# Performance work log

Hardware: AMD Instinct MI355X
Metric: run time of the kernel (lower is better)

Reference implementation:

```python
import jax, jax.numpy as jnp
import numpy as np

H = 1024
R = 16


def setup_inputs() -> dict:
    key = jax.random.key(0)
    ks = jax.random.split(key, 9)
    s = 1.0 / np.sqrt(H)
    x = jax.random.normal(ks[0], (8192, H), dtype=jnp.float32)
    # gate (rule_attention): Linear(H, R)
    Wa = jax.random.uniform(ks[1], (H, R), minval=-s, maxval=s, dtype=jnp.float32)
    ba = jax.random.uniform(ks[2], (R,), minval=-s, maxval=s, dtype=jnp.float32)
    # stacked rule_heads: R x (Linear(H,H) -> ReLU -> Linear(H,H))
    W1 = jax.random.uniform(ks[3], (R, H, H), minval=-s, maxval=s, dtype=jnp.float32)
    b1 = jax.random.uniform(ks[4], (R, H), minval=-s, maxval=s, dtype=jnp.float32)
    W2 = jax.random.uniform(ks[5], (R, H, H), minval=-s, maxval=s, dtype=jnp.float32)
    b2 = jax.random.uniform(ks[6], (R, H), minval=-s, maxval=s, dtype=jnp.float32)
    # stacked rule_confidence: R x (Linear(H,1) -> Sigmoid)
    Wc = jax.random.uniform(ks[7], (R, H), minval=-s, maxval=s, dtype=jnp.float32)
    bc = jax.random.uniform(ks[8], (R,), minval=-s, maxval=s, dtype=jnp.float32)
    return {"x": x, "Wa": Wa, "ba": ba, "W1": W1, "b1": b1,
            "W2": W2, "b2": b2, "Wc": Wc, "bc": bc}


def reference(x, Wa, ba, W1, b1, W2, b2, Wc, bc):
    # gate: softmax over rules               [B, R]
    attention = jax.nn.softmax(x @ Wa + ba, axis=-1)
    # all rule MLPs as one batched matmul    [B, R, H]
    h = jax.nn.relu(jnp.einsum("bh,rhd->brd", x, W1) + b1)
    outputs = jnp.einsum("brd,rdo->bro", h, W2) + b2
    # per-rule confidence                    [B, R]
    confidences = jax.nn.sigmoid(jnp.einsum("bh,rh->br", x, Wc) + bc)
    # combine gate with confidence, renormalize, weighted sum over rules
    combined = attention * confidences
    combined = combined / (combined.sum(axis=-1, keepdims=True) + 1e-8)
    output = jnp.einsum("bro,br->bo", outputs, combined)  # [B, H]
    return output, confidences
```

## Files before the change

kernel.cpp:

```cpp
#include <hip/hip_runtime.h>

typedef __attribute__((ext_vector_type(8))) short short8;
typedef __attribute__((ext_vector_type(4))) float f32x4;

#define B_SZ 8192
#define H_SZ 1024
#define R_SZ 16

__device__ __forceinline__ unsigned short f2bf(float f) {
  union { float f; unsigned u; } v; v.f = f;
  unsigned u = v.u + 0x7FFFu + ((v.u >> 16) & 1u);
  return (unsigned short)(u >> 16);
}

__global__ __launch_bounds__(256) void tck_transpose(const float* __restrict__ src,
                                                     unsigned short* __restrict__ dst,
                                                     int rows, int cols) {
  __shared__ float t[32][33];
  size_t zoff = (size_t)blockIdx.z * (size_t)rows * cols;
  int c0 = blockIdx.x * 32, r0 = blockIdx.y * 32;
  int tx = threadIdx.x, ty = threadIdx.y;
#pragma unroll
  for (int i = 0; i < 4; ++i)
    t[ty + 8 * i][tx] = src[zoff + (size_t)(r0 + ty + 8 * i) * cols + c0 + tx];
  __syncthreads();
#pragma unroll
  for (int i = 0; i < 4; ++i)
    dst[zoff + (size_t)(c0 + ty + 8 * i) * rows + r0 + tx] = f2bf(t[tx][ty + 8 * i]);
}

__global__ __launch_bounds__(256) void twk_transpose_wa(const float* __restrict__ Wa,
                                                        float* __restrict__ WaT) {
  int t = blockIdx.x * 256 + threadIdx.x;
  int h = t >> 4, r = t & 15;
  WaT[r * H_SZ + h] = Wa[t];
}

__global__ __launch_bounds__(256) void gk_gate(const float* __restrict__ x,
                                               const float* __restrict__ WaT,
                                               const float* __restrict__ ba,
                                               const float* __restrict__ Wc,
                                               const float* __restrict__ bc,
                                               float* __restrict__ comb,
                                               float* __restrict__ conf,
                                               unsigned short* __restrict__ xb) {
  int b = blockIdx.x * 4 + (threadIdx.x >> 6);
  int l = threadIdx.x & 63;
  const float* xr = x + (size_t)b * H_SZ;
  unsigned short* xbr = xb + (size_t)b * H_SZ;
  float xv[16];
#pragma unroll
  for (int j = 0; j < 16; ++j) xv[j] = xr[l + 64 * j];
#pragma unroll
  for (int j = 0; j < 16; ++j) xbr[l + 64 * j] = f2bf(xv[j]);
  float la[16], lcf[16];
#pragma unroll
  for (int r = 0; r < 16; ++r) {
    float sa = 0.f, sc = 0.f;
#pragma unroll
    for (int j = 0; j < 16; ++j) {
      int h = l + 64 * j;
      sa += xv[j] * WaT[r * H_SZ + h];
      sc += xv[j] * Wc[r * H_SZ + h];
    }
#pragma unroll
    for (int off = 32; off > 0; off >>= 1) {
      sa += __shfl_xor(sa, off);
      sc += __shfl_xor(sc, off);
    }
    la[r] = sa + ba[r];
    lcf[r] = sc + bc[r];
  }
  float mx = la[0];
#pragma unroll
  for (int r = 1; r < 16; ++r) mx = fmaxf(mx, la[r]);
  float se = 0.f;
#pragma unroll
  for (int r = 0; r < 16; ++r) { la[r] = expf(la[r] - mx); se += la[r]; }
  float cb[16]; float cs = 0.f;
#pragma unroll
  for (int r = 0; r < 16; ++r) {
    float cf = 1.f / (1.f + expf(-lcf[r]));
    lcf[r] = cf;
    cb[r] = (la[r] / se) * cf;
    cs += cb[r];
  }
  float inv = 1.f / (cs + 1e-8f);
  if (l < 16) {
    float cv = 0.f, qv = 0.f;
#pragma unroll
    for (int r = 0; r < 16; ++r)
      if (r == l) { cv = lcf[r]; qv = cb[r] * inv; }
    conf[b * 16 + l] = cv;
    comb[b * 16 + l] = qv;
  }
}

__device__ __forceinline__ void gload16(const unsigned short* g, const unsigned short* l) {
  __builtin_amdgcn_global_load_lds(
      (const __attribute__((address_space(1))) unsigned int*)g,
      (__attribute__((address_space(3))) unsigned int*)(unsigned short*)l, 16, 0, 0);
}

#define RDA(DST, MH)                                                                   \
  _Pragma("unroll") for (int c = 0; c < 2; ++c)                                        \
  _Pragma("unroll") for (int f = 0; f < 4; ++f) {                                      \
    int ra = (MH) * 128 + wm * 64 + f * 16 + lc;                                       \
    DST[c][f] = *(const short8*)(bufp + ra * 64 + (((c * 4 + lr) ^ (ra & 7)) * 8));    \
  }
#define RDB(DST, NH)                                                                   \
  _Pragma("unroll") for (int c = 0; c < 2; ++c)                                        \
  _Pragma("unroll") for (int g = 0; g < 2; ++g) {                                      \
    int rb = (NH) * 128 + wn * 32 + g * 16 + lc;                                       \
    DST[c][g] = *(const short8*)(bufp + ABM + rb * 64 + (((c * 4 + lr) ^ (rb & 7)) * 8)); \
  }
#define MF(AS, BS, MH, NH)                                                             \
  __builtin_amdgcn_s_setprio(1);                                                       \
  _Pragma("unroll") for (int c = 0; c < 2; ++c)                                        \
  _Pragma("unroll") for (int f = 0; f < 4; ++f)                                        \
  _Pragma("unroll") for (int g = 0; g < 2; ++g)                                        \
    acc[(MH) * 4 + f][(NH) * 2 + g] = __builtin_amdgcn_mfma_f32_16x16x32_bf16(         \
        AS[c][f], BS[c][g], acc[(MH) * 4 + f][(NH) * 2 + g], 0, 0, 0);                 \
  __builtin_amdgcn_s_setprio(0);
#define LGKM0                                                                          \
  asm volatile("s_waitcnt lgkmcnt(0)" ::: "memory");                                   \
  __builtin_amdgcn_sched_barrier(0);

template <int MODE>
__global__ __launch_bounds__(512, 1) void g1k_gemm8(
    const unsigned short* __restrict__ A, int lda,
    const unsigned short* __restrict__ Bm, int ldb, int K,
    unsigned short* __restrict__ Hp, int ldh,
    const float* __restrict__ b1v,
    float* __restrict__ Out,
    const float* __restrict__ b2v,
    const float* __restrict__ comb,
    int r_base, int accum) {
  constexpr int ABM = 256 * 64;
  constexpr int BUFE = 2 * ABM;
  __shared__ unsigned short smem[2 * BUFE];

  const int tid = threadIdx.x;
  const int lane = tid & 63;
  const int wid = tid >> 6;
  const int wm = wid >> 2, wn = wid & 3;
  const int lr = lane >> 4, lc = lane & 15;
  const int bn0 = blockIdx.x * 256;
  const int bm0 = blockIdx.y * 256;
  const int KT = K >> 6;

  f32x4 acc[8][4];
#pragma unroll
  for (int i = 0; i < 8; ++i)
#pragma unroll
    for (int j = 0; j < 4; ++j) acc[i][j] = {0.f, 0.f, 0.f, 0.f};

  auto stageA = [&](int buf, int kt, int h) {
#pragma unroll
    for (int q = 0; q < 2; ++q) {
      int idx = q * 512 + tid;
      int row = h * 128 + (idx >> 3);
      int ck = (idx & 7) ^ (row & 7);
      gload16(A + (size_t)(bm0 + row) * lda + kt * 64 + ck * 8,
              smem + buf * BUFE + h * 8192 + (q * 512 + (tid & ~63)) * 8);
    }
  };
  auto stageB = [&](int buf, int kt, int h) {
#pragma unroll
    for (int q = 0; q < 2; ++q) {
      int idx = q * 512 + tid;
      int row = h * 128 + (idx >> 3);
      int ck = (idx & 7) ^ (row & 7);
      gload16(Bm + (size_t)(bn0 + row) * ldb + kt * 64 + ck * 8,
              smem + buf * BUFE + ABM + h * 8192 + (q * 512 + (tid & ~63)) * 8);
    }
  };

  stageA(0, 0, 0); stageB(0, 0, 0); stageB(0, 0, 1); stageA(0, 0, 1);
  stageA(1, 1, 0); stageB(1, 1, 0); stageB(1, 1, 1);
  asm volatile("s_waitcnt vmcnt(6)" ::: "memory");
  __builtin_amdgcn_s_barrier();

  for (int t = 0; t < KT; ++t) {
    const unsigned short* bufp = smem + (t & 1) * BUFE;
    const int nb = (t & 1) ^ 1;
    const int cb = (t & 1);
    short8 a0[2][4], a1[2][4], b0[2][2], b1h[2][2];

    RDA(a0, 0)
    RDB(b0, 0)
    if (t + 1 < KT) stageA(nb, t + 1, 1);
    __builtin_amdgcn_s_barrier();
    LGKM0
    MF(a0, b0, 0, 0)
    __builtin_amdgcn_s_barrier();

    RDB(b1h, 1)
    if (t + 2 < KT) stageA(cb, t + 2, 0);
    __builtin_amdgcn_s_barrier();
    LGKM0
    MF(a0, b1h, 0, 1)
    __builtin_amdgcn_s_barrier();

    RDA(a1, 1)
    if (t + 2 < KT) stageB(cb, t + 2, 0);
    __builtin_amdgcn_s_barrier();
    LGKM0
    MF(a1, b1h, 1, 1)
    __builtin_amdgcn_s_barrier();

    if (t + 2 < KT) stageB(cb, t + 2, 1);
    __builtin_amdgcn_s_barrier();
    MF(a1, b0, 1, 0)
    asm volatile("s_waitcnt vmcnt(6)" ::: "memory");
    __builtin_amdgcn_s_barrier();
  }

#pragma unroll
  for (int i = 0; i < 8; ++i) {
#pragma unroll
    for (int j = 0; j < 4; ++j) {
      int m0 = bm0 + (i >> 2) * 128 + wm * 64 + (i & 3) * 16 + lr * 4;
      int n = bn0 + (j >> 1) * 128 + wn * 32 + (j & 1) * 16 + lc;
      f32x4 a = acc[i][j];
      if (MODE == 0) {
        int r = r_base + (n >> 10);
        int d = n & 1023;
        float bias = b1v[r * H_SZ + d];
#pragma unroll
        for (int jj = 0; jj < 4; ++jj) {
          float v = fmaxf(a[jj] + bias, 0.f) * comb[(size_t)(m0 + jj) * 16 + r];
          Hp[(size_t)(m0 + jj) * ldh + n] = f2bf(v);
        }
      } else {
#pragma unroll
        for (int jj = 0; jj < 4; ++jj) {
          size_t row = (size_t)(m0 + jj);
          float v = a[jj];
          if (accum) {
            v += Out[row * H_SZ + n];
          } else {
            float bs = 0.f;
#pragma unroll
            for (int r = 0; r < 16; ++r)
              bs += comb[row * 16 + r] * b2v[r * H_SZ + n];
            v += bs;
          }
          Out[row * H_SZ + n] = v;
        }
      }
    }
  }
}
#undef RDA
#undef RDB
#undef MF
#undef LGKM0

__global__ __launch_bounds__(256) void g2s_gemm(
    const unsigned short* __restrict__ A, int lda,
    const unsigned short* __restrict__ B, int ldb,
    int K,
    float* __restrict__ Out,
    const float* __restrict__ b2v,
    const float* __restrict__ comb,
    int accum) {
  __shared__ short smem[16384];
  short* As = smem;
  short* Bs = smem + 8192;

  const int tid = threadIdx.x;
  const int lane = tid & 63;
  const int wid = tid >> 6;
  const int wm = wid >> 1, wn = wid & 1;
  const int lr = lane >> 4, lc = lane & 15;

  const int id = blockIdx.x;
  const int bm0 = (id & 63) * 128;
  const int bn0 = (id >> 6) * 128;

  int srow[4], ssc[4];
#pragma unroll
  for (int i = 0; i < 4; ++i) {
    int idx = i * 256 + tid;
    srow[i] = idx >> 3;
    ssc[i] = idx & 7;
  }

  const f32x4 zero = {0.f, 0.f, 0.f, 0.f};
  f32x4 acc[4][4];
#pragma unroll
  for (int i = 0; i < 4; ++i)
#pragma unroll
    for (int j = 0; j < 4; ++j) acc[i][j] = zero;

  const int KT = K >> 6;

  short8 va[4], vb[4];
#pragma unroll
  for (int i = 0; i < 4; ++i) {
    va[i] = *(const short8*)(A + (size_t)(bm0 + srow[i]) * lda + ssc[i] * 8);
    vb[i] = *(const short8*)(B + (size_t)(bn0 + srow[i]) * ldb + ssc[i] * 8);
  }

  for (int kt = 0; kt < KT; ++kt) {
    __syncthreads();
#pragma unroll
    for (int i = 0; i < 4; ++i) {
      *(short8*)(As + srow[i] * 64 + ((ssc[i] ^ (srow[i] & 7)) * 8)) = va[i];
      *(short8*)(Bs + srow[i] * 64 + ((ssc[i] ^ (srow[i] & 7)) * 8)) = vb[i];
    }
    __syncthreads();
    if (kt + 1 < KT) {
      int k0 = (kt + 1) << 6;
#pragma unroll
      for (int i = 0; i < 4; ++i) {
        va[i] = *(const short8*)(A + (size_t)(bm0 + srow[i]) * lda + k0 + ssc[i] * 8);
        vb[i] = *(const short8*)(B + (size_t)(bn0 + srow[i]) * ldb + k0 + ssc[i] * 8);
      }
    }
#pragma unroll
    for (int c = 0; c < 2; ++c) {
      short8 af[4], bfr[4];
#pragma unroll
      for (int f = 0; f < 4; ++f) {
        int ra = wm * 64 + f * 16 + lc;
        af[f] = *(const short8*)(As + ra * 64 + (((c * 4 + lr) ^ (ra & 7)) * 8));
        int rb = wn * 64 + f * 16 + lc;
        bfr[f] = *(const short8*)(Bs + rb * 64 + (((c * 4 + lr) ^ (rb & 7)) * 8));
      }
#pragma unroll
      for (int mf = 0; mf < 4; ++mf)
#pragma unroll
        for (int nf = 0; nf < 4; ++nf)
          acc[mf][nf] = __builtin_amdgcn_mfma_f32_16x16x32_bf16(af[mf], bfr[nf],
                                                                acc[mf][nf], 0, 0, 0);
    }
  }

#pragma unroll
  for (int mf = 0; mf < 4; ++mf) {
#pragma unroll
    for (int nf = 0; nf < 4; ++nf) {
      int m0 = bm0 + wm * 64 + mf * 16 + lr * 4;
      int n = bn0 + wn * 64 + nf * 16 + lc;
      f32x4 a = acc[mf][nf];
#pragma unroll
      for (int j = 0; j < 4; ++j) {
        size_t row = (size_t)(m0 + j);
        float v = a[j];
        if (accum) {
          v += Out[row * H_SZ + n];
        } else {
          float bs = 0.f;
#pragma unroll
          for (int r = 0; r < 16; ++r)
            bs += comb[row * 16 + r] * b2v[r * H_SZ + n];
          v += bs;
        }
        Out[row * H_SZ + n] = v;
      }
    }
  }
}

extern "C" void kernel_launch(void* const* d_in, const int* in_sizes, int n_in,
                              void* d_out, int out_size, void* d_ws, size_t ws_size,
                              hipStream_t stream) {
  if (n_in < 9) return;
  const float* x  = (const float*)d_in[0];
  const float* Wa = (const float*)d_in[1];
  const float* ba = (const float*)d_in[2];
  const float* W1 = (const float*)d_in[3];
  const float* b1 = (const float*)d_in[4];
  const float* W2 = (const float*)d_in[5];
  const float* b2 = (const float*)d_in[6];
  const float* Wc = (const float*)d_in[7];
  const float* bc = (const float*)d_in[8];

  float* out = (float*)d_out;
  float* conf = out + (size_t)B_SZ * H_SZ;

  char* w = (char*)d_ws;
  unsigned short* xb = (unsigned short*)w;  w += (size_t)B_SZ * H_SZ * 2;
  unsigned short* W1T = (unsigned short*)w; w += (size_t)R_SZ * H_SZ * H_SZ * 2;
  unsigned short* W2T = (unsigned short*)w; w += (size_t)R_SZ * H_SZ * H_SZ * 2;
  float* comb = (float*)w;                  w += (size_t)B_SZ * R_SZ * 4;
  float* WaT = (float*)w;                   w += (size_t)R_SZ * H_SZ * 4;
  unsigned short* Hp = (unsigned short*)w;
  size_t used = (size_t)(w - (char*)d_ws);

  int G = 16;
  while (G > 1 && used + (size_t)B_SZ * G * H_SZ * 2 > ws_size) G >>= 1;
  if (used + (size_t)B_SZ * G * H_SZ * 2 > ws_size) return;

  dim3 tb(32, 8);
  tck_transpose<<<dim3(32, 32, 16), tb, 0, stream>>>(W1, W1T, H_SZ, H_SZ);
  tck_transpose<<<dim3(32, 512, 1), tb, 0, stream>>>(W2, W2T, R_SZ * H_SZ, H_SZ);
  twk_transpose_wa<<<dim3(64), dim3(256), 0, stream>>>(Wa, WaT);
  gk_gate<<<dim3(B_SZ / 4), dim3(256), 0, stream>>>(x, WaT, ba, Wc, bc, comb, conf, xb);

  int ngroups = R_SZ / G;
  for (int g = 0; g < ngroups; ++g) {
    g1k_gemm8<0><<<dim3(G * H_SZ / 256, B_SZ / 256), dim3(512), 0, stream>>>(
        xb, H_SZ,
        W1T + (size_t)g * G * H_SZ * H_SZ, H_SZ, H_SZ,
        Hp, G * H_SZ, b1, nullptr, nullptr, comb, g * G, 0);
    g2s_gemm<<<dim3(512), dim3(256), 0, stream>>>(
        Hp, G * H_SZ,
        W2T + (size_t)g * G * H_SZ, R_SZ * H_SZ, G * H_SZ,
        out, b2, comb, (g > 0) ? 1 : 0);
  }
}
```

Measured before the change: 702.7 us.

## Use split-K big-tile GEMM for second layer with partial-sum reduction

Replaces the second-layer g2s_gemm with a MODE 2 instance of the large 256x256 MFMA kernel that splits the K dimension in two across blockIdx.z. One half writes into the output and the other into a separate fp32 partial buffer, which a new elementwise kernel adds afterwards. The goal is to fill the GPU with more blocks (32x4x2 = 256 instead of 128 large tiles) while reusing the faster pipelined kernel. The cost is an extra workspace buffer, an extra read-modify-write pass over the 32 MB output, and fp32 summation order changes. If the workspace is too small it falls back to the old path.

```diff
diff --git a/kernel.cpp b/kernel.cpp
--- a/kernel.cpp
+++ b/kernel.cpp
@@ -96,6 +96,15 @@
   }
 }
 
+__global__ __launch_bounds__(256) void redk_add(float* __restrict__ out,
+                                                const float* __restrict__ p1) {
+  size_t i = ((size_t)blockIdx.x * 256 + threadIdx.x) * 4;
+  float4 a = *(const float4*)(out + i);
+  float4 b = *(const float4*)(p1 + i);
+  a.x += b.x; a.y += b.y; a.z += b.z; a.w += b.w;
+  *(float4*)(out + i) = a;
+}
+
 __device__ __forceinline__ void gload16(const unsigned short* g, const unsigned short* l) {
   __builtin_amdgcn_global_load_lds(
       (const __attribute__((address_space(1))) unsigned int*)g,
@@ -135,7 +144,8 @@
     float* __restrict__ Out,
     const float* __restrict__ b2v,
     const float* __restrict__ comb,
-    int r_base, int accum) {
+    int r_base, int accum,
+    float* __restrict__ Out2) {
   constexpr int ABM = 256 * 64;
   constexpr int BUFE = 2 * ABM;
   __shared__ unsigned short smem[2 * BUFE];
@@ -145,9 +155,13 @@
   const int wid = tid >> 6;
   const int wm = wid >> 2, wn = wid & 3;
   const int lr = lane >> 4, lc = lane & 15;
-  const int bn0 = blockIdx.x * 256;
-  const int bm0 = blockIdx.y * 256;
+  const int bn0 = (MODE == 2 ? blockIdx.y : blockIdx.x) * 256;
+  const int bm0 = (MODE == 2 ? blockIdx.x : blockIdx.y) * 256;
   const int KT = K >> 6;
+  if (MODE == 2) {
+    A += (size_t)blockIdx.z * (size_t)K;
+    Bm += (size_t)blockIdx.z * (size_t)K;
+  }
 
   f32x4 acc[8][4];
 #pragma unroll
@@ -233,20 +247,21 @@
           Hp[(size_t)(m0 + jj) * ldh + n] = f2bf(v);
         }
       } else {
+        float* dst = blockIdx.z ? Out2 : Out;
 #pragma unroll
         for (int jj = 0; jj < 4; ++jj) {
           size_t row = (size_t)(m0 + jj);
           float v = a[jj];
           if (accum) {
-            v += Out[row * H_SZ + n];
-          } else {
+            v += dst[row * H_SZ + n];
+          } else if (blockIdx.z == 0) {
             float bs = 0.f;
 #pragma unroll
             for (int r = 0; r < 16; ++r)
               bs += comb[row * 16 + r] * b2v[r * H_SZ + n];
             v += bs;
           }
-          Out[row * H_SZ + n] = v;
+          dst[row * H_SZ + n] = v;
         }
       }
     }
@@ -394,6 +409,10 @@
   while (G > 1 && used + (size_t)B_SZ * G * H_SZ * 2 > ws_size) G >>= 1;
   if (used + (size_t)B_SZ * G * H_SZ * 2 > ws_size) return;
 
+  char* afterHp = (char*)Hp + (size_t)B_SZ * G * H_SZ * 2;
+  float* part1 = (float*)afterHp;
+  bool splitk = ((size_t)(afterHp - (char*)d_ws) + (size_t)B_SZ * H_SZ * 4 <= ws_size);
+
   dim3 tb(32, 8);
   tck_transpose<<<dim3(32, 32, 16), tb, 0, stream>>>(W1, W1T, H_SZ, H_SZ);
   tck_transpose<<<dim3(32, 512, 1), tb, 0, stream>>>(W2, W2T, R_SZ * H_SZ, H_SZ);
@@ -405,10 +424,19 @@
     g1k_gemm8<0><<<dim3(G * H_SZ / 256, B_SZ / 256), dim3(512), 0, stream>>>(
         xb, H_SZ,
         W1T + (size_t)g * G * H_SZ * H_SZ, H_SZ, H_SZ,
-        Hp, G * H_SZ, b1, nullptr, nullptr, comb, g * G, 0);
-    g2s_gemm<<<dim3(512), dim3(256), 0, stream>>>(
-        Hp, G * H_SZ,
-        W2T + (size_t)g * G * H_SZ, R_SZ * H_SZ, G * H_SZ,
-        out, b2, comb, (g > 0) ? 1 : 0);
-  }
-}
+        Hp, G * H_SZ, b1, nullptr, nullptr, comb, g * G, 0, nullptr);
+    if (splitk) {
+      g1k_gemm8<2><<<dim3(B_SZ / 256, H_SZ / 256, 2), dim3(512), 0, stream>>>(
+          Hp, G * H_SZ,
+          W2T + (size_t)g * G * H_SZ, R_SZ * H_SZ, (G * H_SZ) / 2,
+          nullptr, 0, nullptr, out, b2, comb, 0, (g > 0) ? 1 : 0, part1);
+    } else {
+      g2s_gemm<<<dim3(512), dim3(256), 0, stream>>>(
+          Hp, G * H_SZ,
+          W2T + (size_t)g * G * H_SZ, R_SZ * H_SZ, G * H_SZ,
+          out, b2, comb, (g > 0) ? 1 : 0);
+    }
+  }
+  if (splitk)
+    redk_add<<<dim3((B_SZ * H_SZ) / (256 * 4)), dim3(256), 0, stream>>>(out, part1);
+}
```

New measurement: 826.1 us. +17.6%, slower.
